# Performance work log

Measured on AMD Instinct MI355X. Metric: run time of the kernel, lower is better.

The kernel has to match this reference:

```python
import jax, jax.numpy as jnp
import numpy as np

B, C, T = 8, 8, 2048
WIN = 512
F_BINS = WIN // 2 + 1  # 257
H, NH = 256, 4
DH = H // NH
EPS = 1e-4


def _ln(x, g, b):
    m = jnp.mean(x, -1, keepdims=True)
    v = jnp.var(x, -1, keepdims=True)
    return (x - m) / jnp.sqrt(v + 1e-5) * g + b


def setup_inputs() -> dict:
    key = jax.random.key(0)
    ks = jax.random.split(key, 16)
    w = lambda i, shape: jax.random.normal(ks[i], shape, jnp.float32) * 0.02
    return {
        'x': jax.random.normal(ks[0], (B, C, T, F_BINS), jnp.float32),
        'W_in': w(1, (F_BINS, H)), 'b_in': jnp.zeros((H,), jnp.float32),
        'W_out': w(2, (H, F_BINS)), 'b_out': jnp.zeros((F_BINS,), jnp.float32),
        'Wq': w(3, (H, H)), 'bq': jnp.zeros((H,), jnp.float32),
        'Wk': w(4, (H, H)), 'bk': jnp.zeros((H,), jnp.float32),
        'Wv': w(5, (H, H)), 'bv': jnp.zeros((H,), jnp.float32),
        'Wo': w(6, (H, H)), 'bo': jnp.zeros((H,), jnp.float32),
        'ln1_g': jnp.ones((H,), jnp.float32), 'ln1_b': jnp.zeros((H,), jnp.float32),
        'Wf1': w(7, (H, WIN)), 'bf1': jnp.zeros((WIN,), jnp.float32),
        'Wf2': w(8, (WIN, H)), 'bf2': jnp.zeros((H,), jnp.float32),
        'ln2_g': jnp.ones((H,), jnp.float32), 'ln2_b': jnp.zeros((H,), jnp.float32),
        'Ws1': w(9, (H, H // 2)), 'bs1': jnp.zeros((H // 2,), jnp.float32),
        'Ws2': w(10, (H // 2, 1)), 'bs2': jnp.zeros((1,), jnp.float32),
        'ps_a': jnp.zeros((1,), jnp.float32), 'ps_b': jnp.ones((1,), jnp.float32),
    }


def _forward(x, W_in, b_in, W_out, b_out, Wq, bq, Wk, bk, Wv, bv, Wo, bo,
             ln1_g, ln1_b, Wf1, bf1, Wf2, bf2, ln2_g, ln2_b,
             Ws1, bs1, Ws2, bs2, ps_a, ps_b):
    lin1 = jax.nn.relu(x @ W_in + b_in)  # [B,C,T,H]
    b, c, t, h_dim = lin1.shape

    def encoder(q, kv):
        # q: [B,T,H], kv: [B,Cc,T,H]; per-time-frame attention over channels
        cc = kv.shape[1]
        Q = (q @ Wq + bq).reshape(b, t, NH, DH)
        K = (kv @ Wk + bk).reshape(b, cc, t, NH, DH)
        V = (kv @ Wv + bv).reshape(b, cc, t, NH, DH)
        scores = jnp.einsum('bthd,bcthd->bthc', Q, K) / jnp.sqrt(jnp.float32(DH))
        A = jax.nn.softmax(scores, axis=-1)
        ctx = jnp.einsum('bthc,bcthd->bthd', A, V).reshape(b, t, h_dim)
        h1 = _ln(q + ctx @ Wo + bo, ln1_g, ln1_b)
        f = jax.nn.relu(h1 @ Wf1 + bf1) @ Wf2 + bf2
        return _ln(h1 + f, ln2_g, ln2_b)

    def seen_enough(hh):
        s = jax.nn.relu(hh @ Ws1 + bs1) @ Ws2 + bs2
        return jax.nn.sigmoid((s - ps_a) / (ps_b + 1e-8))

    still = jnp.ones((b, t, 1), jnp.float32)
    cum = jnp.zeros((b, t, 1), jnp.float32)
    rem = jnp.ones((b, t, 1), jnp.float32)
    pc = jnp.zeros((b, t, 1), jnp.float32)
    out = jnp.zeros((b, t, h_dim), jnp.float32)
    gate = jnp.float32(1.0)  # replicates data-dependent early break

    for ci in range(c):  # small fixed loop over mic channels (ACT ponder)
        hh = encoder(lin1[:, ci], lin1[:, :ci + 1])
        cur = seen_enough(hh) if ci < c - 1 else jnp.ones((b, t, 1), jnp.float32)
        cum_n = cum + cur * still
        pc_n = pc + still
        still_n = (cum_n < 1 - EPS).astype(jnp.float32)
        out_n = out + hh * (cur * still_n + rem * (1 - still_n))
        rem_n = rem - cur * still_n
        pc_n = pc_n + rem_n * (1 - still_n)
        live = gate > 0.5
        cum = jnp.where(live, cum_n, cum)
        pc = jnp.where(live, pc_n, pc)
        out = jnp.where(live, out_n, out)
        rem = jnp.where(live, rem_n, rem)
        still = jnp.where(live, still_n, still)
        gate = gate * (jnp.sum(still) >= EPS).astype(jnp.float32)

    encoder_out = jax.nn.relu(out @ W_out + b_out)  # [B,T,F]
    return encoder_out, pc[:, :, 0]


def reference(x, W_in, b_in, W_out, b_out, Wq, bq, Wk, bk, Wv, bv, Wo, bo,
              ln1_g, ln1_b, Wf1, bf1, Wf2, bf2, ln2_g, ln2_b,
              Ws1, bs1, Ws2, bs2, ps_a, ps_b):
    return _forward(x, W_in, b_in, W_out, b_out, Wq, bq, Wk, bk, Wv, bv, Wo, bo,
                    ln1_g, ln1_b, Wf1, bf1, Wf2, bf2, ln2_g, ln2_b,
                    Ws1, bs1, Ws2, bs2, ps_a, ps_b)
```

## Files before the change

### kernel.cpp

```cpp
#include <hip/hip_runtime.h>
#include <hip/hip_bf16.h>
#include <math.h>

typedef _Float16 f16;
typedef _Float16 f16x4 __attribute__((ext_vector_type(4)));
typedef _Float16 f16x8 __attribute__((ext_vector_type(8)));
typedef float f32x16 __attribute__((ext_vector_type(16)));

constexpr int CH = 8;
constexpr int TT = 2048;
constexpr int FB = 257;
constexpr int HD = 256;
constexpr int DHD = 64;
constexpr int WN = 512;
constexpr int HF = 128;
constexpr int RR = 8 * TT;
constexpr int KXP = 288;

#define MFMA3(ACCV, AH, AL, BH, BL)                                            \
  ACCV = __builtin_amdgcn_mfma_f32_32x32x16_f16(AL, BH, ACCV, 0, 0, 0);        \
  ACCV = __builtin_amdgcn_mfma_f32_32x32x16_f16(AH, BL, ACCV, 0, 0, 0);        \
  ACCV = __builtin_amdgcn_mfma_f32_32x32x16_f16(AH, BH, ACCV, 0, 0, 0);

template<int ACT>
__global__ __launch_bounds__(256, 2) void gemm2(
    const f16* __restrict__ Ahi, const f16* __restrict__ Alo, int K,
    const f16* __restrict__ Bp, const float* __restrict__ bias,
    float* __restrict__ C0, int ldc, int Nreal)
{
  __shared__ f16 As[2][2][128][40];
  const int tid = threadIdx.x;
  const int m0 = blockIdx.x * 128;
  const int n0 = blockIdx.y * 64;
  const int q = tid & 3, r = tid >> 2;
  const int lane = tid & 63, wm = tid >> 6;
  const int lr = lane & 31, lg = lane >> 5;
  const int nb0 = n0 >> 5, kd8 = K >> 3;

  f32x16 acc[2];
  #pragma unroll
  for (int nf = 0; nf < 2; nf++)
    #pragma unroll
    for (int g = 0; g < 16; g++) acc[nf][g] = 0.f;

  const long aoff = (long)(m0 + r) * K + q * 8;
  const long hstep = (long)64 * K;
  f16x8 sA[4];
  auto loadA = [&](int k0) {
    const long a = aoff + k0;
    sA[0] = *(const f16x8*)(Ahi + a);  sA[1] = *(const f16x8*)(Ahi + a + hstep);
    sA[2] = *(const f16x8*)(Alo + a);  sA[3] = *(const f16x8*)(Alo + a + hstep);
  };
  auto loadB = [&](f16x8 B[2][2][2], int k0) {
    const int kb = (k0 >> 3) + lg;
    #pragma unroll
    for (int kh = 0; kh < 2; kh++)
      #pragma unroll
      for (int nf = 0; nf < 2; nf++)
        #pragma unroll
        for (int hl = 0; hl < 2; hl++)
          B[kh][nf][hl] = *(const f16x8*)(Bp +
              ((long)((nb0 + nf) * kd8 + kb + kh * 2) * 512 + hl * 256 + lr * 8));
  };
  auto kstep = [&](f16x8 SB[2][2][2], f16x8 TB[2][2][2], int k0, int d) {
    *(f16x8*)&As[d][0][r][q * 8]      = sA[0];
    *(f16x8*)&As[d][0][r + 64][q * 8] = sA[1];
    *(f16x8*)&As[d][1][r][q * 8]      = sA[2];
    *(f16x8*)&As[d][1][r + 64][q * 8] = sA[3];
    __syncthreads();
    if (k0 + 32 < K) { loadA(k0 + 32); loadB(TB, k0 + 32); }
    f16x8 fa[2][2];
    #pragma unroll
    for (int kh = 0; kh < 2; kh++)
      #pragma unroll
      for (int hl = 0; hl < 2; hl++)
        fa[kh][hl] = *(const f16x8*)&As[d][hl][wm * 32 + lr][kh * 16 + lg * 8];
    #pragma unroll
    for (int kh = 0; kh < 2; kh++)
      #pragma unroll
      for (int nf = 0; nf < 2; nf++) {
        MFMA3(acc[nf], fa[kh][0], fa[kh][1], SB[kh][nf][0], SB[kh][nf][1]);
      }
  };

  f16x8 B0[2][2][2], B1[2][2][2];
  loadA(0);
  loadB(B0, 0);
  int d = 0;
  for (int k0 = 0; k0 < K; k0 += 64) {
    kstep(B0, B1, k0, d); d ^= 1;
    if (k0 + 32 < K) { kstep(B1, B0, k0 + 32, d); d ^= 1; }
  }

  #pragma unroll
  for (int nf = 0; nf < 2; nf++) {
    const int col = n0 + nf * 32 + lr;
    const float bb = (col < Nreal) ? bias[col] : 0.f;
    #pragma unroll
    for (int g = 0; g < 16; g++) {
      const long row = m0 + wm * 32 + (g & 3) + 8 * (g >> 2) + 4 * lg;
      float v = acc[nf][g] + bb;
      if (ACT) v = fmaxf(v, 0.f);
      if (col < Nreal) C0[row * (long)ldc + col] = v;
    }
  }
}

__global__ __launch_bounds__(512) void lin1_qkv(
    const float* __restrict__ x, long agrp,
    const f16* __restrict__ WinP, const float* __restrict__ b_in,
    const f16* __restrict__ WqkvP, const float* __restrict__ bq,
    const float* __restrict__ bk, const float* __restrict__ bv,
    f16* __restrict__ lin1hi, f16* __restrict__ lin1lo,
    float* __restrict__ Qb, float* __restrict__ Ksd, float* __restrict__ Vsd,
    const int* __restrict__ alive)
{
  if (alive && *alive == 0) return;
  __shared__ f16 As[2][2][64][40];
  __shared__ f16 L1[2][64][264];
  const int tid = threadIdx.x;
  const int m0 = blockIdx.x * 64;
  const int lane = tid & 63, wave = tid >> 6;
  const int wm = wave & 1, wn = wave >> 1;
  const int lr = lane & 31, lg = lane >> 5;
  const int srow = tid >> 3, sk = (tid & 7) * 4;

  const int r0 = m0 + srow;
  const float* xrow = x + (long)(r0 >> 11) * agrp + (long)(r0 & 2047) * FB;

  f16x4 sAh, sAl;
  auto loadA = [&](int k0) {
    float v[4];
    #pragma unroll
    for (int j = 0; j < 4; j++) {
      const int k = k0 + sk + j;
      v[j] = (k < FB) ? xrow[k] : 0.f;
    }
    #pragma unroll
    for (int j = 0; j < 4; j++) {
      const f16 h = (f16)v[j];
      sAh[j] = h; sAl[j] = (f16)(v[j] - (float)h);
    }
  };
  auto loadB1 = [&](f16x8 B[2][2][2], int k0) {
    const int kb = (k0 >> 3) + lg;
    #pragma unroll
    for (int kh = 0; kh < 2; kh++)
      #pragma unroll
      for (int nf = 0; nf < 2; nf++)
        #pragma unroll
        for (int hl = 0; hl < 2; hl++)
          B[kh][nf][hl] = *(const f16x8*)(WinP +
              ((long)((wn * 2 + nf) * 36 + kb + kh * 2) * 512 + hl * 256 + lr * 8));
  };

  f32x16 acc[2];
  #pragma unroll
  for (int nf = 0; nf < 2; nf++)
    #pragma unroll
    for (int g = 0; g < 16; g++) acc[nf][g] = 0.f;

  auto kstep1 = [&](f16x8 SB[2][2][2], f16x8 TB[2][2][2], int k0, int d) {
    *(f16x4*)&As[d][0][srow][sk] = sAh;
    *(f16x4*)&As[d][1][srow][sk] = sAl;
    __syncthreads();
    if (k0 + 32 < KXP) { loadA(k0 + 32); loadB1(TB, k0 + 32); }
    f16x8 fa[2][2];
    #pragma unroll
    for (int kh = 0; kh < 2; kh++)
      #pragma unroll
      for (int hl = 0; hl < 2; hl++)
        fa[kh][hl] = *(const f16x8*)&As[d][hl][wm * 32 + lr][kh * 16 + lg * 8];
    #pragma unroll
    for (int kh = 0; kh < 2; kh++)
      #pragma unroll
      for (int nf = 0; nf < 2; nf++) {
        MFMA3(acc[nf], fa[kh][0], fa[kh][1], SB[kh][nf][0], SB[kh][nf][1]);
      }
  };

  f16x8 B0[2][2][2], B1[2][2][2];
  loadA(0);
  loadB1(B0, 0);
  #pragma unroll
  for (int s = 0; s < 9; s++) {
    if ((s & 1) == 0) kstep1(B0, B1, s * 32, 0);
    else              kstep1(B1, B0, s * 32, 1);
  }

  #pragma unroll
  for (int nf = 0; nf < 2; nf++) {
    const int col = wn * 64 + nf * 32 + lr;
    const float bb = b_in[col];
    #pragma unroll
    for (int g = 0; g < 16; g++) {
      const int row_l = wm * 32 + (g & 3) + 8 * (g >> 2) + 4 * lg;
      const float v = fmaxf(acc[nf][g] + bb, 0.f);
      const f16 hi = (f16)v;
      const f16 lo = (f16)(v - (float)hi);
      L1[0][row_l][col] = hi;
      L1[1][row_l][col] = lo;
      const long gi = (long)(m0 + row_l) * HD + col;
      lin1hi[gi] = hi;
      lin1lo[gi] = lo;
    }
  }
  __syncthreads();

  auto loadB2 = [&](f16x8 B[2][2][2], int k0, int sel) {
    const int kb = (k0 >> 3) + lg;
    #pragma unroll
    for (int kh = 0; kh < 2; kh++)
      #pragma unroll
      for (int nf = 0; nf < 2; nf++)
        #pragma unroll
        for (int hl = 0; hl < 2; hl++)
          B[kh][nf][hl] = *(const f16x8*)(WqkvP +
              ((long)((sel * 8 + wn * 2 + nf) * 32 + kb + kh * 2) * 512 + hl * 256 + lr * 8));
  };
  #pragma unroll
  for (int sel = 0; sel < 3; sel++) {
    f32x16 a2[2];
    #pragma unroll
    for (int nf = 0; nf < 2; nf++)
      #pragma unroll
      for (int g = 0; g < 16; g++) a2[nf][g] = 0.f;
    f16x8 Bc[2][2][2], Bn[2][2][2];
    loadB2(Bc, 0, sel);
    #pragma unroll
    for (int s = 0; s < 8; s++) {
      const int k0 = s * 32;
      if (s < 7) loadB2((s & 1) ? Bc : Bn, k0 + 32, sel);
      f16x8 fa[2][2];
      #pragma unroll
      for (int kh = 0; kh < 2; kh++)
        #pragma unroll
        for (int hl = 0; hl < 2; hl++)
          fa[kh][hl] = *(const f16x8*)&L1[hl][wm * 32 + lr][k0 + kh * 16 + lg * 8];
      #pragma unroll
      for (int kh = 0; kh < 2; kh++)
        #pragma unroll
        for (int nf = 0; nf < 2; nf++) {
          if (s & 1) { MFMA3(a2[nf], fa[kh][0], fa[kh][1], Bn[kh][nf][0], Bn[kh][nf][1]); }
          else       { MFMA3(a2[nf], fa[kh][0], fa[kh][1], Bc[kh][nf][0], Bc[kh][nf][1]); }
        }
    }
    float* dst = sel == 0 ? Qb : (sel == 1 ? Ksd : Vsd);
    const float* bp = sel == 0 ? bq : (sel == 1 ? bk : bv);
    #pragma unroll
    for (int nf = 0; nf < 2; nf++) {
      const int col = wn * 64 + nf * 32 + lr;
      const float bb = bp[col];
      #pragma unroll
      for (int g = 0; g < 16; g++) {
        const int row_l = wm * 32 + (g & 3) + 8 * (g >> 2) + 4 * lg;
        dst[(long)(m0 + row_l) * HD + col] = a2[nf][g] + bb;
      }
    }
  }
}

__global__ __launch_bounds__(512) void ffn_ln(
    const f16* __restrict__ h1hi, const f16* __restrict__ h1lo,
    const f16* __restrict__ Wf1P, const float* __restrict__ bf1,
    const f16* __restrict__ Wf2P, const float* __restrict__ bf2,
    const float* __restrict__ g2, const float* __restrict__ b2,
    f16* __restrict__ hhhi, f16* __restrict__ hhlo,
    const int* __restrict__ alive)
{
  if (alive && *alive == 0) return;
  __shared__ f16 H1[2][64][264];
  __shared__ f16 T1[2][64][264];
  __shared__ float red[64][4][2];
  const int tid = threadIdx.x;
  const int m0 = blockIdx.x * 64;
  const int lane = tid & 63, wave = tid >> 6;
  const int wm = wave & 1, wn = wave >> 1;
  const int lr = lane & 31, lg = lane >> 5;

  {
    const int srow = tid >> 3, scg = (tid & 7) * 32;
    const long hb = (long)(m0 + srow) * HD + scg;
    #pragma unroll
    for (int j = 0; j < 4; j++) {
      *(f16x8*)&H1[0][srow][scg + j * 8] = *(const f16x8*)(h1hi + hb + j * 8);
      *(f16x8*)&H1[1][srow][scg + j * 8] = *(const f16x8*)(h1lo + hb + j * 8);
    }
  }
  __syncthreads();

  auto loadBf1 = [&](f16x8 B[2][2][2], int k0, int p) {
    const int kb = (k0 >> 3) + lg;
    #pragma unroll
    for (int kh = 0; kh < 2; kh++)
      #pragma unroll
      for (int nf = 0; nf < 2; nf++)
        #pragma unroll
        for (int hl = 0; hl < 2; hl++)
          B[kh][nf][hl] = *(const f16x8*)(Wf1P +
              ((long)((p * 8 + wn * 2 + nf) * 32 + kb + kh * 2) * 512 + hl * 256 + lr * 8));
  };
  auto loadBf2 = [&](f16x8 B[2][2][2], int k0, int p) {
    const int kb = p * 32 + (k0 >> 3) + lg;
    #pragma unroll
    for (int kh = 0; kh < 2; kh++)
      #pragma unroll
      for (int nf = 0; nf < 2; nf++)
        #pragma unroll
        for (int hl = 0; hl < 2; hl++)
          B[kh][nf][hl] = *(const f16x8*)(Wf2P +
              ((long)((wn * 2 + nf) * 64 + kb + kh * 2) * 512 + hl * 256 + lr * 8));
  };

  f32x16 hacc[2];
  #pragma unroll
  for (int nf = 0; nf < 2; nf++)
    #pragma unroll
    for (int g = 0; g < 16; g++) hacc[nf][g] = 0.f;

  #pragma unroll
  for (int p = 0; p < 2; p++) {
    f32x16 ta[2];
    #pragma unroll
    for (int nf = 0; nf < 2; nf++)
      #pragma unroll
      for (int g = 0; g < 16; g++) ta[nf][g] = 0.f;
    {
      f16x8 Bc[2][2][2], Bn[2][2][2];
      loadBf1(Bc, 0, p);
      #pragma unroll
      for (int s = 0; s < 8; s++) {
        const int k0 = s * 32;
        if (s < 7) loadBf1((s & 1) ? Bc : Bn, k0 + 32, p);
        f16x8 fa[2][2];
        #pragma unroll
        for (int kh = 0; kh < 2; kh++)
          #pragma unroll
          for (int hl = 0; hl < 2; hl++)
            fa[kh][hl] = *(const f16x8*)&H1[hl][wm * 32 + lr][k0 + kh * 16 + lg * 8];
        #pragma unroll
        for (int kh = 0; kh < 2; kh++)
          #pragma unroll
          for (int nf = 0; nf < 2; nf++) {
            if (s & 1) { MFMA3(ta[nf], fa[kh][0], fa[kh][1], Bn[kh][nf][0], Bn[kh][nf][1]); }
            else       { MFMA3(ta[nf], fa[kh][0], fa[kh][1], Bc[kh][nf][0], Bc[kh][nf][1]); }
          }
      }
    }
    __syncthreads();
    #pragma unroll
    for (int nf = 0; nf < 2; nf++) {
      const int col = wn * 64 + nf * 32 + lr;
      const float bb = bf1[p * 256 + col];
      #pragma unroll
      for (int g = 0; g < 16; g++) {
        const int row_l = wm * 32 + (g & 3) + 8 * (g >> 2) + 4 * lg;
        const float v = fmaxf(ta[nf][g] + bb, 0.f);
        const f16 hi = (f16)v;
        T1[0][row_l][col] = hi;
        T1[1][row_l][col] = (f16)(v - (float)hi);
      }
    }
    __syncthreads();
    {
      f16x8 Bc[2][2][2], Bn[2][2][2];
      loadBf2(Bc, 0, p);
      #pragma unroll
      for (int s = 0; s < 8; s++) {
        const int k0 = s * 32;
        if (s < 7) loadBf2((s & 1) ? Bc : Bn, k0 + 32, p);
        f16x8 ft[2][2];
        #pragma unroll
        for (int kh = 0; kh < 2; kh++)
          #pragma unroll
          for (int hl = 0; hl < 2; hl++)
            ft[kh][hl] = *(const f16x8*)&T1[hl][wm * 32 + lr][k0 + kh * 16 + lg * 8];
        #pragma unroll
        for (int kh = 0; kh < 2; kh++)
          #pragma unroll
          for (int nf = 0; nf < 2; nf++) {
            if (s & 1) { MFMA3(hacc[nf], ft[kh][0], ft[kh][1], Bn[kh][nf][0], Bn[kh][nf][1]); }
            else       { MFMA3(hacc[nf], ft[kh][0], ft[kh][1], Bc[kh][nf][0], Bc[kh][nf][1]); }
          }
      }
    }
  }

  float pr[16], qr[16];
  #pragma unroll
  for (int g = 0; g < 16; g++) {
    const int row_l = wm * 32 + (g & 3) + 8 * (g >> 2) + 4 * lg;
    float s = 0.f, sq = 0.f;
    #pragma unroll
    for (int nf = 0; nf < 2; nf++) {
      const int col = wn * 64 + nf * 32 + lr;
      float v = hacc[nf][g] + bf2[col]
              + (float)H1[0][row_l][col] + (float)H1[1][row_l][col];
      hacc[nf][g] = v;
      s += v; sq += v * v;
    }
    pr[g] = s; qr[g] = sq;
  }
  #pragma unroll
  for (int g = 0; g < 16; g++)
    #pragma unroll
    for (int i = 1; i <= 16; i <<= 1) {
      pr[g] += __shfl_xor(pr[g], i, 64);
      qr[g] += __shfl_xor(qr[g], i, 64);
    }
  if (lr == 0) {
    #pragma unroll
    for (int g = 0; g < 16; g++) {
      const int row_l = wm * 32 + (g & 3) + 8 * (g >> 2) + 4 * lg;
      red[row_l][wn][0] = pr[g];
      red[row_l][wn][1] = qr[g];
    }
  }
  __syncthreads();
  #pragma unroll
  for (int g = 0; g < 16; g++) {
    const int row_l = wm * 32 + (g & 3) + 8 * (g >> 2) + 4 * lg;
    const float mean = (red[row_l][0][0] + red[row_l][1][0] +
                        red[row_l][2][0] + red[row_l][3][0]) * (1.f / HD);
    const float ex2 = (red[row_l][0][1] + red[row_l][1][1] +
                       red[row_l][2][1] + red[row_l][3][1]) * (1.f / HD);
    const float inv = 1.f / sqrtf(ex2 - mean * mean + 1e-5f);
    const long rbase = (long)(m0 + row_l) * HD;
    #pragma unroll
    for (int nf = 0; nf < 2; nf++) {
      const int col = wn * 64 + nf * 32 + lr;
      const float o = (hacc[nf][g] - mean) * inv * g2[col] + b2[col];
      const f16 hi = (f16)o;
      hhhi[rbase + col] = hi;
      hhlo[rbase + col] = (f16)(o - (float)hi);
    }
  }
}

__global__ __launch_bounds__(512) void gemm_ln(
    const f16* __restrict__ Ahi, const f16* __restrict__ Alo, int K,
    const f16* __restrict__ Bp, const float* __restrict__ bias,
    const f16* __restrict__ Rhi, const f16* __restrict__ Rlo,
    const float* __restrict__ gg, const float* __restrict__ bb_,
    f16* __restrict__ Ohi, f16* __restrict__ Olo,
    const int* __restrict__ alive)
{
  if (alive && *alive == 0) return;
  __shared__ f16 As[2][2][64][40];
  __shared__ float red[64][4][2];
  const int tid = threadIdx.x;
  const int m0 = blockIdx.x * 64;
  const int lane = tid & 63, wave = tid >> 6;
  const int wm = wave & 1, wn = wave >> 1;
  const int lr = lane & 31, lg = lane >> 5;
  const int srow = tid >> 3, sk = (tid & 7) * 4;
  const int kd8 = K >> 3;

  f32x16 acc[2];
  #pragma unroll
  for (int nf = 0; nf < 2; nf++)
    #pragma unroll
    for (int g = 0; g < 16; g++) acc[nf][g] = 0.f;

  const f16* arh = Ahi + (long)(m0 + srow) * K + sk;
  const f16* arl = Alo + (long)(m0 + srow) * K + sk;
  f16x4 sAh, sAl;
  auto loadA = [&](int k0) {
    sAh = *(const f16x4*)(arh + k0);
    sAl = *(const f16x4*)(arl + k0);
  };
  auto loadB = [&](f16x8 B[2][2][2], int k0) {
    const int kb = (k0 >> 3) + lg;
    #pragma unroll
    for (int kh = 0; kh < 2; kh++)
      #pragma unroll
      for (int nf = 0; nf < 2; nf++)
        #pragma unroll
        for (int hl = 0; hl < 2; hl++)
          B[kh][nf][hl] = *(const f16x8*)(Bp +
              ((long)((wn * 2 + nf) * kd8 + kb + kh * 2) * 512 + hl * 256 + lr * 8));
  };
  auto kstep = [&](f16x8 SB[2][2][2], f16x8 TB[2][2][2], int k0, int d) {
    *(f16x4*)&As[d][0][srow][sk] = sAh;
    *(f16x4*)&As[d][1][srow][sk] = sAl;
    __syncthreads();
    if (k0 + 32 < K) { loadA(k0 + 32); loadB(TB, k0 + 32); }
    f16x8 fa[2][2];
    #pragma unroll
    for (int kh = 0; kh < 2; kh++)
      #pragma unroll
      for (int hl = 0; hl < 2; hl++)
        fa[kh][hl] = *(const f16x8*)&As[d][hl][wm * 32 + lr][kh * 16 + lg * 8];
    #pragma unroll
    for (int kh = 0; kh < 2; kh++)
      #pragma unroll
      for (int nf = 0; nf < 2; nf++) {
        MFMA3(acc[nf], fa[kh][0], fa[kh][1], SB[kh][nf][0], SB[kh][nf][1]);
      }
  };

  f16x8 B0[2][2][2], B1[2][2][2];
  loadA(0);
  loadB(B0, 0);
  int d = 0;
  for (int k0 = 0; k0 < K; k0 += 64) {
    kstep(B0, B1, k0, d); d ^= 1;
    if (k0 + 32 < K) { kstep(B1, B0, k0 + 32, d); d ^= 1; }
  }

  float pr[16], qr[16];
  #pragma unroll
  for (int g = 0; g < 16; g++) {
    const int row_l = wm * 32 + (g & 3) + 8 * (g >> 2) + 4 * lg;
    const long rbase = (long)(m0 + row_l) * HD;
    float s = 0.f, sq = 0.f;
    #pragma unroll
    for (int nf = 0; nf < 2; nf++) {
      const int col = wn * 64 + nf * 32 + lr;
      float v = acc[nf][g] + bias[col]
              + (float)Rhi[rbase + col] + (float)Rlo[rbase + col];
      acc[nf][g] = v;
      s += v; sq += v * v;
    }
    pr[g] = s; qr[g] = sq;
  }
  #pragma unroll
  for (int g = 0; g < 16; g++)
    #pragma unroll
    for (int i = 1; i <= 16; i <<= 1) {
      pr[g] += __shfl_xor(pr[g], i, 64);
      qr[g] += __shfl_xor(qr[g], i, 64);
    }
  if (lr == 0) {
    #pragma unroll
    for (int g = 0; g < 16; g++) {
      const int row_l = wm * 32 + (g & 3) + 8 * (g >> 2) + 4 * lg;
      red[row_l][wn][0] = pr[g];
      red[row_l][wn][1] = qr[g];
    }
  }
  __syncthreads();
  #pragma unroll
  for (int g = 0; g < 16; g++) {
    const int row_l = wm * 32 + (g & 3) + 8 * (g >> 2) + 4 * lg;
    const float mean = (red[row_l][0][0] + red[row_l][1][0] +
                        red[row_l][2][0] + red[row_l][3][0]) * (1.f / HD);
    const float ex2 = (red[row_l][0][1] + red[row_l][1][1] +
                       red[row_l][2][1] + red[row_l][3][1]) * (1.f / HD);
    const float inv = 1.f / sqrtf(ex2 - mean * mean + 1e-5f);
    const long rbase = (long)(m0 + row_l) * HD;
    #pragma unroll
    for (int nf = 0; nf < 2; nf++) {
      const int col = wn * 64 + nf * 32 + lr;
      const float o = (acc[nf][g] - mean) * inv * gg[col] + bb_[col];
      const f16 hi = (f16)o;
      Ohi[rbase + col] = hi;
      Olo[rbase + col] = (f16)(o - (float)hi);
    }
  }
}

template<int FIRST>
__global__ __launch_bounds__(256) void s1_act(
    const f16* __restrict__ hhhi, const f16* __restrict__ hhlo,
    const f16* __restrict__ Bp, const float* __restrict__ bs1,
    const float* __restrict__ Ws2, const float* __restrict__ bs2,
    const float* __restrict__ psa, const float* __restrict__ psb,
    float* __restrict__ cum, float* __restrict__ rem,
    float* __restrict__ still, float* __restrict__ pc,
    f16* __restrict__ outhi, f16* __restrict__ outlo,
    float* __restrict__ pcdst,
    const int* __restrict__ alive, int* __restrict__ myFlag)
{
  if (!FIRST && alive && *alive == 0) return;
  __shared__ f16 As[2][2][64][40];
  __shared__ float red[64][2];
  const int tid = threadIdx.x;
  const int m0 = blockIdx.x * 64;
  const int lane = tid & 63, wave = tid >> 6;
  const int wm = wave & 1, wn = wave >> 1;
  const int lr = lane & 31, lg = lane >> 5;
  const int srow = tid >> 2, sk = (tid & 3) * 8;
  const int K = HD, kd8 = K >> 3;

  f32x16 acc[2];
  #pragma unroll
  for (int nf = 0; nf < 2; nf++)
    #pragma unroll
    for (int g = 0; g < 16; g++) acc[nf][g] = 0.f;

  const f16* arh = hhhi + (long)(m0 + srow) * K + sk;
  const f16* arl = hhlo + (long)(m0 + srow) * K + sk;
  f16x8 sAh, sAl;
  auto loadA = [&](int k0) {
    sAh = *(const f16x8*)(arh + k0);
    sAl = *(const f16x8*)(arl + k0);
  };
  auto loadB = [&](f16x8 B[2][2][2], int k0) {
    const int kb = (k0 >> 3) + lg;
    #pragma unroll
    for (int kh = 0; kh < 2; kh++)
      #pragma unroll
      for (int nf = 0; nf < 2; nf++)
        #pragma unroll
        for (int hl = 0; hl < 2; hl++)
          B[kh][nf][hl] = *(const f16x8*)(Bp +
              ((long)((wn * 2 + nf) * kd8 + kb + kh * 2) * 512 + hl * 256 + lr * 8));
  };
  auto kstep = [&](f16x8 SB[2][2][2], f16x8 TB[2][2][2], int k0, int d) {
    *(f16x8*)&As[d][0][srow][sk] = sAh;
    *(f16x8*)&As[d][1][srow][sk] = sAl;
    __syncthreads();
    if (k0 + 32 < K) { loadA(k0 + 32); loadB(TB, k0 + 32); }
    f16x8 fa[2][2];
    #pragma unroll
    for (int kh = 0; kh < 2; kh++)
      #pragma unroll
      for (int hl = 0; hl < 2; hl++)
        fa[kh][hl] = *(const f16x8*)&As[d][hl][wm * 32 + lr][kh * 16 + lg * 8];
    #pragma unroll
    for (int kh = 0; kh < 2; kh++)
      #pragma unroll
      for (int nf = 0; nf < 2; nf++) {
        MFMA3(acc[nf], fa[kh][0], fa[kh][1], SB[kh][nf][0], SB[kh][nf][1]);
      }
  };

  f16x8 B0[2][2][2], B1[2][2][2];
  loadA(0);
  loadB(B0, 0);
  int d = 0;
  for (int k0 = 0; k0 < K; k0 += 64) {
    kstep(B0, B1, k0, d); d ^= 1;
    if (k0 + 32 < K) { kstep(B1, B0, k0 + 32, d); d ^= 1; }
  }

  float pr[16];
  #pragma unroll
  for (int g = 0; g < 16; g++) {
    float s = 0.f;
    #pragma unroll
    for (int nf = 0; nf < 2; nf++) {
      const int col = wn * 64 + nf * 32 + lr;
      const float v = fmaxf(acc[nf][g] + bs1[col], 0.f);
      s += v * Ws2[col];
    }
    pr[g] = s;
  }
  #pragma unroll
  for (int g = 0; g < 16; g++)
    #pragma unroll
    for (int i = 1; i <= 16; i <<= 1) pr[g] += __shfl_xor(pr[g], i, 64);
  if (lr == 0) {
    #pragma unroll
    for (int g = 0; g < 16; g++) {
      const int row_l = wm * 32 + (g & 3) + 8 * (g >> 2) + 4 * lg;
      red[row_l][wn] = pr[g];
    }
  }
  __syncthreads();

  const float ipsb = 1.f / (psb[0] + 1e-8f);
  const float pa = psa[0], b2v = bs2[0];
  for (int row_l = 0; row_l < 64; row_l++) {
    const long rg = m0 + row_l;
    const float s = red[row_l][0] + red[row_l][1] + b2v;
    const float curv = 1.f / (1.f + expf(-(s - pa) * ipsb));
    const float cu = FIRST ? 0.f : cum[rg];
    const float re = FIRST ? 1.f : rem[rg];
    const float st = FIRST ? 1.f : still[rg];
    const float pp = FIRST ? 0.f : pc[rg];
    const float cum_n = cu + curv * st;
    float pc_n = pp + st;
    const float still_n = (cum_n < 0.9999f) ? 1.f : 0.f;
    const float wgt = curv * still_n + re * (1.f - still_n);
    const long idx = rg * HD + tid;
    const float prev = FIRST ? 0.f : ((float)outhi[idx] + (float)outlo[idx]);
    const float hhv = (float)hhhi[idx] + (float)hhlo[idx];
    const float newv = prev + hhv * wgt;
    const f16 hi = (f16)newv;
    outhi[idx] = hi;
    outlo[idx] = (f16)(newv - (float)hi);
    const float rem_n = re - curv * still_n;
    pc_n += rem_n * (1.f - still_n);
    if (tid == 0) {
      cum[rg] = cum_n; rem[rg] = rem_n; still[rg] = still_n; pc[rg] = pc_n;
      pcdst[rg] = pc_n;
      if (still_n > 0.5f) *myFlag = 1;
    }
  }
}

__global__ __launch_bounds__(256) void act_last(
    const f16* __restrict__ hhhi, const f16* __restrict__ hhlo,
    float* __restrict__ cum, float* __restrict__ rem,
    float* __restrict__ still, float* __restrict__ pc,
    f16* __restrict__ outhi, f16* __restrict__ outlo,
    float* __restrict__ pcdst, const int* __restrict__ alive)
{
  if (alive && *alive == 0) return;
  const int tid = threadIdx.x;
  for (int rr = 0; rr < 8; rr++) {
    const long r = (long)blockIdx.x * 8 + rr;
    const float re = rem[r], st = still[r];
    const float cum_n = cum[r] + st;
    float pc_n = pc[r] + st;
    const float still_n = (cum_n < 0.9999f) ? 1.f : 0.f;
    const float wgt = still_n + re * (1.f - still_n);
    const long idx = r * HD + tid;
    const float newv = (float)outhi[idx] + (float)outlo[idx]
                     + ((float)hhhi[idx] + (float)hhlo[idx]) * wgt;
    const f16 hi = (f16)newv;
    outhi[idx] = hi;
    outlo[idx] = (f16)(newv - (float)hi);
    const float rem_n = re - still_n;
    pc_n += rem_n * (1.f - still_n);
    if (tid == 0) {
      cum[r] = cum_n; rem[r] = rem_n; still[r] = still_n; pc[r] = pc_n;
      pcdst[r] = pc_n;
    }
  }
}

__global__ __launch_bounds__(256) void wsplit_k(
    const float* __restrict__ W_in, const float* __restrict__ Wq,
    const float* __restrict__ Wk, const float* __restrict__ Wv,
    const float* __restrict__ Wo, const float* __restrict__ Wf1,
    const float* __restrict__ Wf2, const float* __restrict__ Ws1,
    const float* __restrict__ Wout,
    f16* __restrict__ WinP, f16* __restrict__ WqkvP, f16* __restrict__ WoP,
    f16* __restrict__ Wf1P, f16* __restrict__ Wf2P, f16* __restrict__ Ws1P,
    f16* __restrict__ WoutP)
{
  const int y = blockIdx.y;
  const long idx = (long)blockIdx.x * 256 + threadIdx.x;
  int Npad, Kpad, Ksrc;
  f16* dst;
  switch (y) {
    case 0: Npad = 256; Kpad = 288; Ksrc = 257; dst = WinP;  break;
    case 1: Npad = 768; Kpad = 256; Ksrc = 256; dst = WqkvP; break;
    case 2: Npad = 256; Kpad = 256; Ksrc = 256; dst = WoP;   break;
    case 3: Npad = 512; Kpad = 256; Ksrc = 256; dst = Wf1P;  break;
    case 4: Npad = 256; Kpad = 512; Ksrc = 512; dst = Wf2P;  break;
    case 5: Npad = 128; Kpad = 256; Ksrc = 256; dst = Ws1P;  break;
    default: Npad = 384; Kpad = 256; Ksrc = 256; dst = WoutP; break;
  }
  if (idx >= (long)Npad * Kpad) return;
  const int n = (int)(idx / Kpad), k = (int)(idx % Kpad);
  float v = 0.f;
  if (k < Ksrc) {
    switch (y) {
      case 0: v = W_in[(long)k * 256 + n]; break;
      case 1: { const int sel = n >> 8;
                const float* s = sel == 0 ? Wq : (sel == 1 ? Wk : Wv);
                v = s[(long)k * 256 + (n & 255)]; } break;
      case 2: v = Wo[(long)k * 256 + n]; break;
      case 3: v = Wf1[(long)k * 512 + n]; break;
      case 4: v = Wf2[(long)k * 256 + n]; break;
      case 5: v = Ws1[(long)k * 128 + n]; break;
      default: v = (n < 257) ? Wout[(long)k * 257 + n] : 0.f; break;
    }
  }
  const long base = ((long)(n >> 5) * (Kpad >> 3) + (k >> 3)) * 512 + (n & 31) * 8 + (k & 7);
  const f16 hi = (f16)v;
  dst[base] = hi;
  dst[base + 256] = (f16)(v - (float)hi);
}

template<int NCc>
__global__ __launch_bounds__(256) void attn_k(
    const float* __restrict__ Q, const float* __restrict__ Ksp,
    const float* __restrict__ Vsp, f16* __restrict__ chi,
    f16* __restrict__ clo, const int* __restrict__ alive)
{
  if (alive && *alive == 0) return;
  const int w = threadIdx.x >> 6;
  const int l = threadIdx.x & 63;
  for (int rr = 0; rr < 4; rr++) {
    const long r = (long)blockIdx.x * 4 + rr;
    const float qv = Q[r * HD + w * DHD + l];
    float sc[NCc];
    #pragma unroll
    for (int c = 0; c < NCc; c++) {
      float p = qv * Ksp[((long)c * RR + r) * HD + w * DHD + l];
      #pragma unroll
      for (int s = 32; s > 0; s >>= 1) p += __shfl_xor(p, s, 64);
      sc[c] = p * 0.125f;
    }
    float m = sc[0];
    #pragma unroll
    for (int c = 1; c < NCc; c++) m = fmaxf(m, sc[c]);
    float a[NCc];
    float den = 0.f;
    #pragma unroll
    for (int c = 0; c < NCc; c++) { a[c] = expf(sc[c] - m); den += a[c]; }
    float cv = 0.f;
    #pragma unroll
    for (int c = 0; c < NCc; c++)
      cv = fmaf(a[c] / den, Vsp[((long)c * RR + r) * HD + w * DHD + l], cv);
    const f16 hi = (f16)cv;
    chi[r * HD + w * DHD + l] = hi;
    clo[r * HD + w * DHD + l] = (f16)(cv - (float)hi);
  }
}

__global__ void init_k(int* flags) {
  if (threadIdx.x < 8) flags[threadIdx.x] = 0;
}

extern "C" void kernel_launch(void* const* d_in, const int* in_sizes, int n_in,
                              void* d_out, int out_size, void* d_ws, size_t ws_size,
                              hipStream_t stream) {
  const float* x    = (const float*)d_in[0];
  const float* W_in = (const float*)d_in[1];
  const float* b_in = (const float*)d_in[2];
  const float* W_out= (const float*)d_in[3];
  const float* b_out= (const float*)d_in[4];
  const float* Wq   = (const float*)d_in[5];
  const float* bq   = (const float*)d_in[6];
  const float* Wk   = (const float*)d_in[7];
  const float* bk   = (const float*)d_in[8];
  const float* Wv   = (const float*)d_in[9];
  const float* bv   = (const float*)d_in[10];
  const float* Wo   = (const float*)d_in[11];
  const float* bo   = (const float*)d_in[12];
  const float* ln1g = (const float*)d_in[13];
  const float* ln1b = (const float*)d_in[14];
  const float* Wf1  = (const float*)d_in[15];
  const float* bf1  = (const float*)d_in[16];
  const float* Wf2  = (const float*)d_in[17];
  const float* bf2  = (const float*)d_in[18];
  const float* ln2g = (const float*)d_in[19];
  const float* ln2b = (const float*)d_in[20];
  const float* Ws1  = (const float*)d_in[21];
  const float* bs1  = (const float*)d_in[22];
  const float* Ws2  = (const float*)d_in[23];
  const float* bs2  = (const float*)d_in[24];
  const float* psa  = (const float*)d_in[25];
  const float* psb  = (const float*)d_in[26];

  float* ws = (float*)d_ws;
  long off = 0;
  auto alloc = [&](long n) { float* p = ws + off; off += n; return p; };
  float* Ks   = alloc((long)CH * RR * HD);
  float* Vs   = alloc((long)CH * RR * HD);
  float* Qb   = alloc((long)RR * HD);
  f16* lin1hi = (f16*)alloc((long)RR * HD / 2);
  f16* lin1lo = (f16*)alloc((long)RR * HD / 2);
  f16* ctxhi  = (f16*)alloc((long)RR * HD / 2);
  f16* ctxlo  = (f16*)alloc((long)RR * HD / 2);
  f16* h1hi   = (f16*)alloc((long)RR * HD / 2);
  f16* h1lo   = (f16*)alloc((long)RR * HD / 2);
  f16* hhhi   = (f16*)alloc((long)RR * HD / 2);
  f16* hhlo   = (f16*)alloc((long)RR * HD / 2);
  f16* outhi  = (f16*)alloc((long)RR * HD / 2);
  f16* outlo  = (f16*)alloc((long)RR * HD / 2);
  f16* WinP   = (f16*)alloc(2 * 256 * 288 / 2);
  f16* WqkvP  = (f16*)alloc(2 * 768 * 256 / 2);
  f16* WoP    = (f16*)alloc(2 * 256 * 256 / 2);
  f16* Wf1P   = (f16*)alloc(2 * 512 * 256 / 2);
  f16* Wf2P   = (f16*)alloc(2 * 256 * 512 / 2);
  f16* Ws1P   = (f16*)alloc(2 * 128 * 256 / 2);
  f16* WoutP  = (f16*)alloc(2 * 384 * 256 / 2);
  float* cum  = alloc(RR);
  float* rem  = alloc(RR);
  float* still= alloc(RR);
  float* pc   = alloc(RR);
  int* flags  = (int*)alloc(8);

  init_k<<<1, 256, 0, stream>>>(flags);
  wsplit_k<<<dim3(768, 7), 256, 0, stream>>>(
      W_in, Wq, Wk, Wv, Wo, Wf1, Wf2, Ws1, W_out,
      WinP, WqkvP, WoP, Wf1P, Wf2P, Ws1P, WoutP);

  float* pcdst = (float*)d_out + (long)RR * FB;

  for (int ci = 0; ci < CH; ci++) {
    const int* al = (ci == 0) ? nullptr : (flags + ci - 1);
    lin1_qkv<<<256, 512, 0, stream>>>(
        x + (long)ci * TT * FB, (long)CH * TT * FB,
        WinP, b_in, WqkvP, bq, bk, bv,
        lin1hi, lin1lo, Qb,
        Ks + (long)ci * RR * HD, Vs + (long)ci * RR * HD, al);
    switch (ci) {
      case 0: attn_k<1><<<4096, 256, 0, stream>>>(Qb, Ks, Vs, ctxhi, ctxlo, al); break;
      case 1: attn_k<2><<<4096, 256, 0, stream>>>(Qb, Ks, Vs, ctxhi, ctxlo, al); break;
      case 2: attn_k<3><<<4096, 256, 0, stream>>>(Qb, Ks, Vs, ctxhi, ctxlo, al); break;
      case 3: attn_k<4><<<4096, 256, 0, stream>>>(Qb, Ks, Vs, ctxhi, ctxlo, al); break;
      case 4: attn_k<5><<<4096, 256, 0, stream>>>(Qb, Ks, Vs, ctxhi, ctxlo, al); break;
      case 5: attn_k<6><<<4096, 256, 0, stream>>>(Qb, Ks, Vs, ctxhi, ctxlo, al); break;
      case 6: attn_k<7><<<4096, 256, 0, stream>>>(Qb, Ks, Vs, ctxhi, ctxlo, al); break;
      default: attn_k<8><<<4096, 256, 0, stream>>>(Qb, Ks, Vs, ctxhi, ctxlo, al); break;
    }
    gemm_ln<<<256, 512, 0, stream>>>(
        ctxhi, ctxlo, HD, WoP, bo, lin1hi, lin1lo, ln1g, ln1b,
        h1hi, h1lo, al);
    ffn_ln<<<256, 512, 0, stream>>>(
        h1hi, h1lo, Wf1P, bf1, Wf2P, bf2, ln2g, ln2b, hhhi, hhlo, al);
    if (ci == 0)
      s1_act<1><<<256, 256, 0, stream>>>(
          hhhi, hhlo, Ws1P, bs1, Ws2, bs2, psa, psb,
          cum, rem, still, pc, outhi, outlo, pcdst, nullptr, flags + 0);
    else if (ci < CH - 1)
      s1_act<0><<<256, 256, 0, stream>>>(
          hhhi, hhlo, Ws1P, bs1, Ws2, bs2, psa, psb,
          cum, rem, still, pc, outhi, outlo, pcdst, al, flags + ci);
    else
      act_last<<<2048, 256, 0, stream>>>(
          hhhi, hhlo, cum, rem, still, pc, outhi, outlo, pcdst, al);
  }
  gemm2<1><<<dim3(128, 6), 256, 0, stream>>>(
      outhi, outlo, HD, WoutP, b_out, (float*)d_out, FB, FB);
}
```

Before: 749.7 us.

## Fuse attention into Wo+LN kernel and FFN+LN into the halting-score kernel

Attention over channels is now computed inside the Wo projection kernel and written straight to shared memory, so the ctx hi/lo buffers and their global round trip are gone. The FFN+LayerNorm kernel is merged with the halting-score GEMM and accumulation step, and keeps the hh result in shared memory instead of writing and rereading hhhi/hhlo. This removes two to three launches per channel iteration and several activation round trips. The cost is that attention runs only 256 blocks with a serial 32-row loop per wave, and the larger fused kernels may raise register and LDS pressure.

New measurement: 811.9 us. +8.3%, slower.

```diff
diff --git a/kernel.cpp b/kernel.cpp
--- a/kernel.cpp
+++ b/kernel.cpp
@@ -260,36 +260,71 @@
   }
 }
 
-__global__ __launch_bounds__(512) void ffn_ln(
-    const f16* __restrict__ h1hi, const f16* __restrict__ h1lo,
-    const f16* __restrict__ Wf1P, const float* __restrict__ bf1,
-    const f16* __restrict__ Wf2P, const float* __restrict__ bf2,
-    const float* __restrict__ g2, const float* __restrict__ b2,
-    f16* __restrict__ hhhi, f16* __restrict__ hhlo,
+template<int NCc>
+__global__ __launch_bounds__(512) void attn_wo_ln(
+    const float* __restrict__ Qb, const float* __restrict__ Ksp,
+    const float* __restrict__ Vsp,
+    const f16* __restrict__ WoP, const float* __restrict__ bo,
+    const f16* __restrict__ Rhi, const f16* __restrict__ Rlo,
+    const float* __restrict__ gg, const float* __restrict__ bb_,
+    f16* __restrict__ Ohi, f16* __restrict__ Olo,
     const int* __restrict__ alive)
 {
   if (alive && *alive == 0) return;
-  __shared__ f16 H1[2][64][264];
-  __shared__ f16 T1[2][64][264];
+  __shared__ f16 C1[2][64][264];
   __shared__ float red[64][4][2];
   const int tid = threadIdx.x;
   const int m0 = blockIdx.x * 64;
   const int lane = tid & 63, wave = tid >> 6;
+
+  {
+    const int h = wave & 3;
+    const int rbase = (wave >> 2) * 32;
+    for (int i = 0; i < 32; i++) {
+      const int row_l = rbase + i;
+      const long r = m0 + row_l;
+      const long qi = r * HD + h * DHD + lane;
+      const float qv = Qb[qi];
+      float kv[NCc], vv[NCc];
+      #pragma unroll
+      for (int c = 0; c < NCc; c++) {
+        kv[c] = Ksp[((long)c * RR + r) * HD + h * DHD + lane];
+        vv[c] = Vsp[((long)c * RR + r) * HD + h * DHD + lane];
+      }
+      float sc[NCc];
+      #pragma unroll
+      for (int c = 0; c < NCc; c++) {
+        float p = qv * kv[c];
+        #pragma unroll
+        for (int s = 32; s > 0; s >>= 1) p += __shfl_xor(p, s, 64);
+        sc[c] = p * 0.125f;
+      }
+      float m = sc[0];
+      #pragma unroll
+      for (int c = 1; c < NCc; c++) m = fmaxf(m, sc[c]);
+      float a[NCc];
+      float den = 0.f;
+      #pragma unroll
+      for (int c = 0; c < NCc; c++) { a[c] = expf(sc[c] - m); den += a[c]; }
+      float cv = 0.f;
+      #pragma unroll
+      for (int c = 0; c < NCc; c++) cv = fmaf(a[c] / den, vv[c], cv);
+      const f16 hi = (f16)cv;
+      C1[0][row_l][h * DHD + lane] = hi;
+      C1[1][row_l][h * DHD + lane] = (f16)(cv - (float)hi);
+    }
+  }
+  __syncthreads();
+
   const int wm = wave & 1, wn = wave >> 1;
   const int lr = lane & 31, lg = lane >> 5;
-
-  {
-    const int srow = tid >> 3, scg = (tid & 7) * 32;
-    const long hb = (long)(m0 + srow) * HD + scg;
-    #pragma unroll
-    for (int j = 0; j < 4; j++) {
-      *(f16x8*)&H1[0][srow][scg + j * 8] = *(const f16x8*)(h1hi + hb + j * 8);
-      *(f16x8*)&H1[1][srow][scg + j * 8] = *(const f16x8*)(h1lo + hb + j * 8);
-    }
-  }
-  __syncthreads();
-
-  auto loadBf1 = [&](f16x8 B[2][2][2], int k0, int p) {
+  f32x16 acc[2];
+  #pragma unroll
+  for (int nf = 0; nf < 2; nf++)
+    #pragma unroll
+    for (int g = 0; g < 16; g++) acc[nf][g] = 0.f;
+
+  auto loadB = [&](f16x8 B[2][2][2], int k0) {
     const int kb = (k0 >> 3) + lg;
     #pragma unroll
     for (int kh = 0; kh < 2; kh++)
@@ -297,106 +332,42 @@
       for (int nf = 0; nf < 2; nf++)
         #pragma unroll
         for (int hl = 0; hl < 2; hl++)
-          B[kh][nf][hl] = *(const f16x8*)(Wf1P +
-              ((long)((p * 8 + wn * 2 + nf) * 32 + kb + kh * 2) * 512 + hl * 256 + lr * 8));
-  };
-  auto loadBf2 = [&](f16x8 B[2][2][2], int k0, int p) {
-    const int kb = p * 32 + (k0 >> 3) + lg;
-    #pragma unroll
-    for (int kh = 0; kh < 2; kh++)
-      #pragma unroll
-      for (int nf = 0; nf < 2; nf++)
-        #pragma unroll
-        for (int hl = 0; hl < 2; hl++)
-          B[kh][nf][hl] = *(const f16x8*)(Wf2P +
-              ((long)((wn * 2 + nf) * 64 + kb + kh * 2) * 512 + hl * 256 + lr * 8));
-  };
-
-  f32x16 hacc[2];
-  #pragma unroll
-  for (int nf = 0; nf < 2; nf++)
-    #pragma unroll
-    for (int g = 0; g < 16; g++) hacc[nf][g] = 0.f;
-
-  #pragma unroll
-  for (int p = 0; p < 2; p++) {
-    f32x16 ta[2];
-    #pragma unroll
-    for (int nf = 0; nf < 2; nf++)
-      #pragma unroll
-      for (int g = 0; g < 16; g++) ta[nf][g] = 0.f;
-    {
-      f16x8 Bc[2][2][2], Bn[2][2][2];
-      loadBf1(Bc, 0, p);
-      #pragma unroll
-      for (int s = 0; s < 8; s++) {
-        const int k0 = s * 32;
-        if (s < 7) loadBf1((s & 1) ? Bc : Bn, k0 + 32, p);
-        f16x8 fa[2][2];
-        #pragma unroll
-        for (int kh = 0; kh < 2; kh++)
-          #pragma unroll
-          for (int hl = 0; hl < 2; hl++)
-            fa[kh][hl] = *(const f16x8*)&H1[hl][wm * 32 + lr][k0 + kh * 16 + lg * 8];
-        #pragma unroll
-        for (int kh = 0; kh < 2; kh++)
-          #pragma unroll
-          for (int nf = 0; nf < 2; nf++) {
-            if (s & 1) { MFMA3(ta[nf], fa[kh][0], fa[kh][1], Bn[kh][nf][0], Bn[kh][nf][1]); }
-            else       { MFMA3(ta[nf], fa[kh][0], fa[kh][1], Bc[kh][nf][0], Bc[kh][nf][1]); }
-          }
-      }
-    }
-    __syncthreads();
+          B[kh][nf][hl] = *(const f16x8*)(WoP +
+              ((long)((wn * 2 + nf) * 32 + kb + kh * 2) * 512 + hl * 256 + lr * 8));
+  };
+  f16x8 Bc[2][2][2], Bn[2][2][2];
+  loadB(Bc, 0);
+  #pragma unroll
+  for (int s = 0; s < 8; s++) {
+    const int k0 = s * 32;
+    if (s < 7) loadB((s & 1) ? Bc : Bn, k0 + 32);
+    f16x8 fa[2][2];
+    #pragma unroll
+    for (int kh = 0; kh < 2; kh++)
+      #pragma unroll
+      for (int hl = 0; hl < 2; hl++)
+        fa[kh][hl] = *(const f16x8*)&C1[hl][wm * 32 + lr][k0 + kh * 16 + lg * 8];
+    #pragma unroll
+    for (int kh = 0; kh < 2; kh++)
+      #pragma unroll
+      for (int nf = 0; nf < 2; nf++) {
+        if (s & 1) { MFMA3(acc[nf], fa[kh][0], fa[kh][1], Bn[kh][nf][0], Bn[kh][nf][1]); }
+        else       { MFMA3(acc[nf], fa[kh][0], fa[kh][1], Bc[kh][nf][0], Bc[kh][nf][1]); }
+      }
+  }
+
+  float pr[16], qr[16];
+  #pragma unroll
+  for (int g = 0; g < 16; g++) {
+    const int row_l = wm * 32 + (g & 3) + 8 * (g >> 2) + 4 * lg;
+    const long rbase = (long)(m0 + row_l) * HD;
+    float s = 0.f, sq = 0.f;
     #pragma unroll
     for (int nf = 0; nf < 2; nf++) {
       const int col = wn * 64 + nf * 32 + lr;
-      const float bb = bf1[p * 256 + col];
-      #pragma unroll
-      for (int g = 0; g < 16; g++) {
-        const int row_l = wm * 32 + (g & 3) + 8 * (g >> 2) + 4 * lg;
-        const float v = fmaxf(ta[nf][g] + bb, 0.f);
-        const f16 hi = (f16)v;
-        T1[0][row_l][col] = hi;
-        T1[1][row_l][col] = (f16)(v - (float)hi);
-      }
-    }
-    __syncthreads();
-    {
-      f16x8 Bc[2][2][2], Bn[2][2][2];
-      loadBf2(Bc, 0, p);
-      #pragma unroll
-      for (int s = 0; s < 8; s++) {
-        const int k0 = s * 32;
-        if (s < 7) loadBf2((s & 1) ? Bc : Bn, k0 + 32, p);
-        f16x8 ft[2][2];
-        #pragma unroll
-        for (int kh = 0; kh < 2; kh++)
-          #pragma unroll
-          for (int hl = 0; hl < 2; hl++)
-            ft[kh][hl] = *(const f16x8*)&T1[hl][wm * 32 + lr][k0 + kh * 16 + lg * 8];
-        #pragma unroll
-        for (int kh = 0; kh < 2; kh++)
-          #pragma unroll
-          for (int nf = 0; nf < 2; nf++) {
-            if (s & 1) { MFMA3(hacc[nf], ft[kh][0], ft[kh][1], Bn[kh][nf][0], Bn[kh][nf][1]); }
-            else       { MFMA3(hacc[nf], ft[kh][0], ft[kh][1], Bc[kh][nf][0], Bc[kh][nf][1]); }
-          }
-      }
-    }
-  }
-
-  float pr[16], qr[16];
-  #pragma unroll
-  for (int g = 0; g < 16; g++) {
-    const int row_l = wm * 32 + (g & 3) + 8 * (g >> 2) + 4 * lg;
-    float s = 0.f, sq = 0.f;
-    #pragma unroll
-    for (int nf = 0; nf < 2; nf++) {
-      const int col = wn * 64 + nf * 32 + lr;
-      float v = hacc[nf][g] + bf2[col]
-              + (float)H1[0][row_l][col] + (float)H1[1][row_l][col];
-      hacc[nf][g] = v;
+      float v = acc[nf][g] + bo[col]
+              + (float)Rhi[rbase + col] + (float)Rlo[rbase + col];
+      acc[nf][g] = v;
       s += v; sq += v * v;
     }
     pr[g] = s; qr[g] = sq;
@@ -429,129 +400,6 @@
     #pragma unroll
     for (int nf = 0; nf < 2; nf++) {
       const int col = wn * 64 + nf * 32 + lr;
-      const float o = (hacc[nf][g] - mean) * inv * g2[col] + b2[col];
-      const f16 hi = (f16)o;
-      hhhi[rbase + col] = hi;
-      hhlo[rbase + col] = (f16)(o - (float)hi);
-    }
-  }
-}
-
-__global__ __launch_bounds__(512) void gemm_ln(
-    const f16* __restrict__ Ahi, const f16* __restrict__ Alo, int K,
-    const f16* __restrict__ Bp, const float* __restrict__ bias,
-    const f16* __restrict__ Rhi, const f16* __restrict__ Rlo,
-    const float* __restrict__ gg, const float* __restrict__ bb_,
-    f16* __restrict__ Ohi, f16* __restrict__ Olo,
-    const int* __restrict__ alive)
-{
-  if (alive && *alive == 0) return;
-  __shared__ f16 As[2][2][64][40];
-  __shared__ float red[64][4][2];
-  const int tid = threadIdx.x;
-  const int m0 = blockIdx.x * 64;
-  const int lane = tid & 63, wave = tid >> 6;
-  const int wm = wave & 1, wn = wave >> 1;
-  const int lr = lane & 31, lg = lane >> 5;
-  const int srow = tid >> 3, sk = (tid & 7) * 4;
-  const int kd8 = K >> 3;
-
-  f32x16 acc[2];
-  #pragma unroll
-  for (int nf = 0; nf < 2; nf++)
-    #pragma unroll
-    for (int g = 0; g < 16; g++) acc[nf][g] = 0.f;
-
-  const f16* arh = Ahi + (long)(m0 + srow) * K + sk;
-  const f16* arl = Alo + (long)(m0 + srow) * K + sk;
-  f16x4 sAh, sAl;
-  auto loadA = [&](int k0) {
-    sAh = *(const f16x4*)(arh + k0);
-    sAl = *(const f16x4*)(arl + k0);
-  };
-  auto loadB = [&](f16x8 B[2][2][2], int k0) {
-    const int kb = (k0 >> 3) + lg;
-    #pragma unroll
-    for (int kh = 0; kh < 2; kh++)
-      #pragma unroll
-      for (int nf = 0; nf < 2; nf++)
-        #pragma unroll
-        for (int hl = 0; hl < 2; hl++)
-          B[kh][nf][hl] = *(const f16x8*)(Bp +
-              ((long)((wn * 2 + nf) * kd8 + kb + kh * 2) * 512 + hl * 256 + lr * 8));
-  };
-  auto kstep = [&](f16x8 SB[2][2][2], f16x8 TB[2][2][2], int k0, int d) {
-    *(f16x4*)&As[d][0][srow][sk] = sAh;
-    *(f16x4*)&As[d][1][srow][sk] = sAl;
-    __syncthreads();
-    if (k0 + 32 < K) { loadA(k0 + 32); loadB(TB, k0 + 32); }
-    f16x8 fa[2][2];
-    #pragma unroll
-    for (int kh = 0; kh < 2; kh++)
-      #pragma unroll
-      for (int hl = 0; hl < 2; hl++)
-        fa[kh][hl] = *(const f16x8*)&As[d][hl][wm * 32 + lr][kh * 16 + lg * 8];
-    #pragma unroll
-    for (int kh = 0; kh < 2; kh++)
-      #pragma unroll
-      for (int nf = 0; nf < 2; nf++) {
-        MFMA3(acc[nf], fa[kh][0], fa[kh][1], SB[kh][nf][0], SB[kh][nf][1]);
-      }
-  };
-
-  f16x8 B0[2][2][2], B1[2][2][2];
-  loadA(0);
-  loadB(B0, 0);
-  int d = 0;
-  for (int k0 = 0; k0 < K; k0 += 64) {
-    kstep(B0, B1, k0, d); d ^= 1;
-    if (k0 + 32 < K) { kstep(B1, B0, k0 + 32, d); d ^= 1; }
-  }
-
-  float pr[16], qr[16];
-  #pragma unroll
-  for (int g = 0; g < 16; g++) {
-    const int row_l = wm * 32 + (g & 3) + 8 * (g >> 2) + 4 * lg;
-    const long rbase = (long)(m0 + row_l) * HD;
-    float s = 0.f, sq = 0.f;
-    #pragma unroll
-    for (int nf = 0; nf < 2; nf++) {
-      const int col = wn * 64 + nf * 32 + lr;
-      float v = acc[nf][g] + bias[col]
-              + (float)Rhi[rbase + col] + (float)Rlo[rbase + col];
-      acc[nf][g] = v;
-      s += v; sq += v * v;
-    }
-    pr[g] = s; qr[g] = sq;
-  }
-  #pragma unroll
-  for (int g = 0; g < 16; g++)
-    #pragma unroll
-    for (int i = 1; i <= 16; i <<= 1) {
-      pr[g] += __shfl_xor(pr[g], i, 64);
-      qr[g] += __shfl_xor(qr[g], i, 64);
-    }
-  if (lr == 0) {
-    #pragma unroll
-    for (int g = 0; g < 16; g++) {
-      const int row_l = wm * 32 + (g & 3) + 8 * (g >> 2) + 4 * lg;
-      red[row_l][wn][0] = pr[g];
-      red[row_l][wn][1] = qr[g];
-    }
-  }
-  __syncthreads();
-  #pragma unroll
-  for (int g = 0; g < 16; g++) {
-    const int row_l = wm * 32 + (g & 3) + 8 * (g >> 2) + 4 * lg;
-    const float mean = (red[row_l][0][0] + red[row_l][1][0] +
-                        red[row_l][2][0] + red[row_l][3][0]) * (1.f / HD);
-    const float ex2 = (red[row_l][0][1] + red[row_l][1][1] +
-                       red[row_l][2][1] + red[row_l][3][1]) * (1.f / HD);
-    const float inv = 1.f / sqrtf(ex2 - mean * mean + 1e-5f);
-    const long rbase = (long)(m0 + row_l) * HD;
-    #pragma unroll
-    for (int nf = 0; nf < 2; nf++) {
-      const int col = wn * 64 + nf * 32 + lr;
       const float o = (acc[nf][g] - mean) * inv * gg[col] + bb_[col];
       const f16 hi = (f16)o;
       Ohi[rbase + col] = hi;
@@ -560,10 +408,13 @@
   }
 }
 
-template<int FIRST>
-__global__ __launch_bounds__(256) void s1_act(
-    const f16* __restrict__ hhhi, const f16* __restrict__ hhlo,
-    const f16* __restrict__ Bp, const float* __restrict__ bs1,
+template<int MODE>
+__global__ __launch_bounds__(512) void ffn_act(
+    const f16* __restrict__ h1hi, const f16* __restrict__ h1lo,
+    const f16* __restrict__ Wf1P, const float* __restrict__ bf1,
+    const f16* __restrict__ Wf2P, const float* __restrict__ bf2,
+    const float* __restrict__ g2, const float* __restrict__ b2,
+    const f16* __restrict__ Ws1P, const float* __restrict__ bs1,
     const float* __restrict__ Ws2, const float* __restrict__ bs2,
     const float* __restrict__ psa, const float* __restrict__ psb,
     float* __restrict__ cum, float* __restrict__ rem,
@@ -572,152 +423,273 @@
     float* __restrict__ pcdst,
     const int* __restrict__ alive, int* __restrict__ myFlag)
 {
-  if (!FIRST && alive && *alive == 0) return;
-  __shared__ f16 As[2][2][64][40];
-  __shared__ float red[64][2];
+  if (MODE != 0 && alive && *alive == 0) return;
+  __shared__ f16 H1[2][64][264];
+  __shared__ f16 T1[2][64][264];
+  __shared__ float red[64][4][2];
+  __shared__ float red2[64][2];
   const int tid = threadIdx.x;
   const int m0 = blockIdx.x * 64;
   const int lane = tid & 63, wave = tid >> 6;
   const int wm = wave & 1, wn = wave >> 1;
   const int lr = lane & 31, lg = lane >> 5;
-  const int srow = tid >> 2, sk = (tid & 3) * 8;
-  const int K = HD, kd8 = K >> 3;
-
-  f32x16 acc[2];
+
+  {
+    const int srow = tid >> 3, scg = (tid & 7) * 32;
+    const long hb = (long)(m0 + srow) * HD + scg;
+    #pragma unroll
+    for (int j = 0; j < 4; j++) {
+      *(f16x8*)&H1[0][srow][scg + j * 8] = *(const f16x8*)(h1hi + hb + j * 8);
+      *(f16x8*)&H1[1][srow][scg + j * 8] = *(const f16x8*)(h1lo + hb + j * 8);
+    }
+  }
+  __syncthreads();
+
+  auto loadBf1 = [&](f16x8 B[2][2][2], int k0, int p) {
+    const int kb = (k0 >> 3) + lg;
+    #pragma unroll
+    for (int kh = 0; kh < 2; kh++)
+      #pragma unroll
+      for (int nf = 0; nf < 2; nf++)
+        #pragma unroll
+        for (int hl = 0; hl < 2; hl++)
+          B[kh][nf][hl] = *(const f16x8*)(Wf1P +
+              ((long)((p * 8 + wn * 2 + nf) * 32 + kb + kh * 2) * 512 + hl * 256 + lr * 8));
+  };
+  auto loadBf2 = [&](f16x8 B[2][2][2], int k0, int p) {
+    const int kb = p * 32 + (k0 >> 3) + lg;
+    #pragma unroll
+    for (int kh = 0; kh < 2; kh++)
+      #pragma unroll
+      for (int nf = 0; nf < 2; nf++)
+        #pragma unroll
+        for (int hl = 0; hl < 2; hl++)
+          B[kh][nf][hl] = *(const f16x8*)(Wf2P +
+              ((long)((wn * 2 + nf) * 64 + kb + kh * 2) * 512 + hl * 256 + lr * 8));
+  };
+
+  f32x16 hacc[2];
   #pragma unroll
   for (int nf = 0; nf < 2; nf++)
     #pragma unroll
-    for (int g = 0; g < 16; g++) acc[nf][g] = 0.f;
-
-  const f16* arh = hhhi + (long)(m0 + srow) * K + sk;
-  const f16* arl = hhlo + (long)(m0 + srow) * K + sk;
-  f16x8 sAh, sAl;
-  auto loadA = [&](int k0) {
-    sAh = *(const f16x8*)(arh + k0);
-    sAl = *(const f16x8*)(arl + k0);
-  };
-  auto loadB = [&](f16x8 B[2][2][2], int k0) {
-    const int kb = (k0 >> 3) + lg;
-    #pragma unroll
-    for (int kh = 0; kh < 2; kh++)
-      #pragma unroll
-      for (int nf = 0; nf < 2; nf++)
-        #pragma unroll
-        for (int hl = 0; hl < 2; hl++)
-          B[kh][nf][hl] = *(const f16x8*)(Bp +
-              ((long)((wn * 2 + nf) * kd8 + kb + kh * 2) * 512 + hl * 256 + lr * 8));
-  };
-  auto kstep = [&](f16x8 SB[2][2][2], f16x8 TB[2][2][2], int k0, int d) {
-    *(f16x8*)&As[d][0][srow][sk] = sAh;
-    *(f16x8*)&As[d][1][srow][sk] = sAl;
+    for (int g = 0; g < 16; g++) hacc[nf][g] = 0.f;
+
+  #pragma unroll
+  for (int p = 0; p < 2; p++) {
+    f32x16 ta[2];
+    #pragma unroll
+    for (int nf = 0; nf < 2; nf++)
+      #pragma unroll
+      for (int g = 0; g < 16; g++) ta[nf][g] = 0.f;
+    {
+      f16x8 Bc[2][2][2], Bn[2][2][2];
+      loadBf1(Bc, 0, p);
+      #pragma unroll
+      for (int s = 0; s < 8; s++) {
+        const int k0 = s * 32;
+        if (s < 7) loadBf1((s & 1) ? Bc : Bn, k0 + 32, p);
+        f16x8 fa[2][2];
+        #pragma unroll
+        for (int kh = 0; kh < 2; kh++)
+          #pragma unroll
+          for (int hl = 0; hl < 2; hl++)
+            fa[kh][hl] = *(const f16x8*)&H1[hl][wm * 32 + lr][k0 + kh * 16 + lg * 8];
+        #pragma unroll
+        for (int kh = 0; kh < 2; kh++)
+          #pragma unroll
+          for (int nf = 0; nf < 2; nf++) {
+            if (s & 1) { MFMA3(ta[nf], fa[kh][0], fa[kh][1], Bn[kh][nf][0], Bn[kh][nf][1]); }
+            else       { MFMA3(ta[nf], fa[kh][0], fa[kh][1], Bc[kh][nf][0], Bc[kh][nf][1]); }
+          }
+      }
+    }
     __syncthreads();
-    if (k0 + 32 < K) { loadA(k0 + 32); loadB(TB, k0 + 32); }
-    f16x8 fa[2][2];
-    #pragma unroll
-    for (int kh = 0; kh < 2; kh++)
-      #pragma unroll
-      for (int hl = 0; hl < 2; hl++)
-        fa[kh][hl] = *(const f16x8*)&As[d][hl][wm * 32 + lr][kh * 16 + lg * 8];
-    #pragma unroll
-    for (int kh = 0; kh < 2; kh++)
-      #pragma unroll
-      for (int nf = 0; nf < 2; nf++) {
-        MFMA3(acc[nf], fa[kh][0], fa[kh][1], SB[kh][nf][0], SB[kh][nf][1]);
-      }
-  };
-
-  f16x8 B0[2][2][2], B1[2][2][2];
-  loadA(0);
-  loadB(B0, 0);
-  int d = 0;
-  for (int k0 = 0; k0 < K; k0 += 64) {
-    kstep(B0, B1, k0, d); d ^= 1;
-    if (k0 + 32 < K) { kstep(B1, B0, k0 + 32, d); d ^= 1; }
-  }
-
-  float pr[16];
-  #pragma unroll
-  for (int g = 0; g < 16; g++) {
-    float s = 0.f;
     #pragma unroll
     for (int nf = 0; nf < 2; nf++) {
       const int col = wn * 64 + nf * 32 + lr;
-      const float v = fmaxf(acc[nf][g] + bs1[col], 0.f);
-      s += v * Ws2[col];
-    }
-    pr[g] = s;
+      const float bb = bf1[p * 256 + col];
+      #pragma unroll
+      for (int g = 0; g < 16; g++) {
+        const int row_l = wm * 32 + (g & 3) + 8 * (g >> 2) + 4 * lg;
+        const float v = fmaxf(ta[nf][g] + bb, 0.f);
+        const f16 hi = (f16)v;
+        T1[0][row_l][col] = hi;
+        T1[1][row_l][col] = (f16)(v - (float)hi);
+      }
+    }
+    __syncthreads();
+    {
+      f16x8 Bc[2][2][2], Bn[2][2][2];
+      loadBf2(Bc, 0, p);
+      #pragma unroll
+      for (int s = 0; s < 8; s++) {
+        const int k0 = s * 32;
+        if (s < 7) loadBf2((s & 1) ? Bc : Bn, k0 + 32, p);
+        f16x8 ft[2][2];
+        #pragma unroll
+        for (int kh = 0; kh < 2; kh++)
+          #pragma unroll
+          for (int hl = 0; hl < 2; hl++)
+            ft[kh][hl] = *(const f16x8*)&T1[hl][wm * 32 + lr][k0 + kh * 16 + lg * 8];
+        #pragma unroll
+        for (int kh = 0; kh < 2; kh++)
+          #pragma unroll
+          for (int nf = 0; nf < 2; nf++) {
+            if (s & 1) { MFMA3(hacc[nf], ft[kh][0], ft[kh][1], Bn[kh][nf][0], Bn[kh][nf][1]); }
+            else       { MFMA3(hacc[nf], ft[kh][0], ft[kh][1], Bc[kh][nf][0], Bc[kh][nf][1]); }
+          }
+      }
+    }
+  }
+
+  float pr[16], qr[16];
+  #pragma unroll
+  for (int g = 0; g < 16; g++) {
+    const int row_l = wm * 32 + (g & 3) + 8 * (g >> 2) + 4 * lg;
+    float s = 0.f, sq = 0.f;
+    #pragma unroll
+    for (int nf = 0; nf < 2; nf++) {
+      const int col = wn * 64 + nf * 32 + lr;
+      float v = hacc[nf][g] + bf2[col]
+              + (float)H1[0][row_l][col] + (float)H1[1][row_l][col];
+      hacc[nf][g] = v;
+      s += v; sq += v * v;
+    }
+    pr[g] = s; qr[g] = sq;
   }
   #pragma unroll
   for (int g = 0; g < 16; g++)
     #pragma unroll
-    for (int i = 1; i <= 16; i <<= 1) pr[g] += __shfl_xor(pr[g], i, 64);
+    for (int i = 1; i <= 16; i <<= 1) {
+      pr[g] += __shfl_xor(pr[g], i, 64);
+      qr[g] += __shfl_xor(qr[g], i, 64);
+    }
   if (lr == 0) {
     #pragma unroll
     for (int g = 0; g < 16; g++) {
       const int row_l = wm * 32 + (g & 3) + 8 * (g >> 2) + 4 * lg;
-      red[row_l][wn] = pr[g];
+      red[row_l][wn][0] = pr[g];
+      red[row_l][wn][1] = qr[g];
+    }
+  }
+  __syncthreads();
+  #pragma unroll
+  for (int g = 0; g < 16; g++) {
+    const int row_l = wm * 32 + (g & 3) + 8 * (g >> 2) + 4 * lg;
+    const float mean = (red[row_l][0][0] + red[row_l][1][0] +
+                        red[row_l][2][0] + red[row_l][3][0]) * (1.f / HD);
+    const float ex2 = (red[row_l][0][1] + red[row_l][1][1] +
+                       red[row_l][2][1] + red[row_l][3][1]) * (1.f / HD);
+    const float inv = 1.f / sqrtf(ex2 - mean * mean + 1e-5f);
+    #pragma unroll
+    for (int nf = 0; nf < 2; nf++) {
+      const int col = wn * 64 + nf * 32 + lr;
+      const float o = (hacc[nf][g] - mean) * inv * g2[col] + b2[col];
+      const f16 hi = (f16)o;
+      T1[0][row_l][col] = hi;
+      T1[1][row_l][col] = (f16)(o - (float)hi);
+    }
+  }
+  __syncthreads();
+
+  if (MODE != 2) {
+    if (wave < 4) {
+      f32x16 sacc[2];
+      #pragma unroll
+      for (int nf = 0; nf < 2; nf++)
+        #pragma unroll
+        for (int g = 0; g < 16; g++) sacc[nf][g] = 0.f;
+      auto loadBs = [&](f16x8 B[2][2][2], int k0) {
+        const int kb = (k0 >> 3) + lg;
+        #pragma unroll
+        for (int kh = 0; kh < 2; kh++)
+          #pragma unroll
+          for (int nf = 0; nf < 2; nf++)
+            #pragma unroll
+            for (int hl = 0; hl < 2; hl++)
+              B[kh][nf][hl] = *(const f16x8*)(Ws1P +
+                  ((long)((wn * 2 + nf) * 32 + kb + kh * 2) * 512 + hl * 256 + lr * 8));
+      };
+      f16x8 Bc[2][2][2], Bn[2][2][2];
+      loadBs(Bc, 0);
+      #pragma unroll
+      for (int s = 0; s < 8; s++) {
+        const int k0 = s * 32;
+        if (s < 7) loadBs((s & 1) ? Bc : Bn, k0 + 32);
+        f16x8 fa[2][2];
+        #pragma unroll
+        for (int kh = 0; kh < 2; kh++)
+          #pragma unroll
+          for (int hl = 0; hl < 2; hl++)
+            fa[kh][hl] = *(const f16x8*)&T1[hl][wm * 32 + lr][k0 + kh * 16 + lg * 8];
+        #pragma unroll
+        for (int kh = 0; kh < 2; kh++)
+          #pragma unroll
+          for (int nf = 0; nf < 2; nf++) {
+            if (s & 1) { MFMA3(sacc[nf], fa[kh][0], fa[kh][1], Bn[kh][nf][0], Bn[kh][nf][1]); }
+            else       { MFMA3(sacc[nf], fa[kh][0], fa[kh][1], Bc[kh][nf][0], Bc[kh][nf][1]); }
+          }
+      }
+      float pr2[16];
+      #pragma unroll
+      for (int g = 0; g < 16; g++) {
+        float s = 0.f;
+        #pragma unroll
+        for (int nf = 0; nf < 2; nf++) {
+          const int col = wn * 64 + nf * 32 + lr;
+          const float v = fmaxf(sacc[nf][g] + bs1[col], 0.f);
+          s += v * Ws2[col];
+        }
+        pr2[g] = s;
+      }
+      #pragma unroll
+      for (int g = 0; g < 16; g++)
+        #pragma unroll
+        for (int i = 1; i <= 16; i <<= 1) pr2[g] += __shfl_xor(pr2[g], i, 64);
+      if (lr == 0) {
+        #pragma unroll
+        for (int g = 0; g < 16; g++) {
+          const int row_l = wm * 32 + (g & 3) + 8 * (g >> 2) + 4 * lg;
+          red2[row_l][wn] = pr2[g];
+        }
+      }
     }
   }
   __syncthreads();
 
   const float ipsb = 1.f / (psb[0] + 1e-8f);
   const float pa = psa[0], b2v = bs2[0];
-  for (int row_l = 0; row_l < 64; row_l++) {
+  const int colA = tid & 255, rsub = tid >> 8;
+  for (int rr = 0; rr < 32; rr++) {
+    const int row_l = rr * 2 + rsub;
     const long rg = m0 + row_l;
-    const float s = red[row_l][0] + red[row_l][1] + b2v;
-    const float curv = 1.f / (1.f + expf(-(s - pa) * ipsb));
-    const float cu = FIRST ? 0.f : cum[rg];
-    const float re = FIRST ? 1.f : rem[rg];
-    const float st = FIRST ? 1.f : still[rg];
-    const float pp = FIRST ? 0.f : pc[rg];
+    float curv;
+    if (MODE == 2) curv = 1.f;
+    else {
+      const float s = red2[row_l][0] + red2[row_l][1] + b2v;
+      curv = 1.f / (1.f + expf(-(s - pa) * ipsb));
+    }
+    const float cu = (MODE == 0) ? 0.f : cum[rg];
+    const float re = (MODE == 0) ? 1.f : rem[rg];
+    const float st = (MODE == 0) ? 1.f : still[rg];
+    const float pp = (MODE == 0) ? 0.f : pc[rg];
     const float cum_n = cu + curv * st;
     float pc_n = pp + st;
     const float still_n = (cum_n < 0.9999f) ? 1.f : 0.f;
     const float wgt = curv * still_n + re * (1.f - still_n);
-    const long idx = rg * HD + tid;
-    const float prev = FIRST ? 0.f : ((float)outhi[idx] + (float)outlo[idx]);
-    const float hhv = (float)hhhi[idx] + (float)hhlo[idx];
+    const long idx = rg * HD + colA;
+    const float prev = (MODE == 0) ? 0.f : ((float)outhi[idx] + (float)outlo[idx]);
+    const float hhv = (float)T1[0][row_l][colA] + (float)T1[1][row_l][colA];
     const float newv = prev + hhv * wgt;
     const f16 hi = (f16)newv;
     outhi[idx] = hi;
     outlo[idx] = (f16)(newv - (float)hi);
     const float rem_n = re - curv * still_n;
     pc_n += rem_n * (1.f - still_n);
-    if (tid == 0) {
+    if (colA == 0) {
       cum[rg] = cum_n; rem[rg] = rem_n; still[rg] = still_n; pc[rg] = pc_n;
       pcdst[rg] = pc_n;
-      if (still_n > 0.5f) *myFlag = 1;
-    }
-  }
-}
-
-__global__ __launch_bounds__(256) void act_last(
-    const f16* __restrict__ hhhi, const f16* __restrict__ hhlo,
-    float* __restrict__ cum, float* __restrict__ rem,
-    float* __restrict__ still, float* __restrict__ pc,
-    f16* __restrict__ outhi, f16* __restrict__ outlo,
-    float* __restrict__ pcdst, const int* __restrict__ alive)
-{
-  if (alive && *alive == 0) return;
-  const int tid = threadIdx.x;
-  for (int rr = 0; rr < 8; rr++) {
-    const long r = (long)blockIdx.x * 8 + rr;
-    const float re = rem[r], st = still[r];
-    const float cum_n = cum[r] + st;
-    float pc_n = pc[r] + st;
-    const float still_n = (cum_n < 0.9999f) ? 1.f : 0.f;
-    const float wgt = still_n + re * (1.f - still_n);
-    const long idx = r * HD + tid;
-    const float newv = (float)outhi[idx] + (float)outlo[idx]
-                     + ((float)hhhi[idx] + (float)hhlo[idx]) * wgt;
-    const f16 hi = (f16)newv;
-    outhi[idx] = hi;
-    outlo[idx] = (f16)(newv - (float)hi);
-    const float rem_n = re - still_n;
-    pc_n += rem_n * (1.f - still_n);
-    if (tid == 0) {
-      cum[r] = cum_n; rem[r] = rem_n; still[r] = still_n; pc[r] = pc_n;
-      pcdst[r] = pc_n;
+      if (MODE != 2 && still_n > 0.5f) *myFlag = 1;
     }
   }
 }
@@ -765,43 +737,6 @@
   const f16 hi = (f16)v;
   dst[base] = hi;
   dst[base + 256] = (f16)(v - (float)hi);
-}
-
-template<int NCc>
-__global__ __launch_bounds__(256) void attn_k(
-    const float* __restrict__ Q, const float* __restrict__ Ksp,
-    const float* __restrict__ Vsp, f16* __restrict__ chi,
-    f16* __restrict__ clo, const int* __restrict__ alive)
-{
-  if (alive && *alive == 0) return;
-  const int w = threadIdx.x >> 6;
-  const int l = threadIdx.x & 63;
-  for (int rr = 0; rr < 4; rr++) {
-    const long r = (long)blockIdx.x * 4 + rr;
-    const float qv = Q[r * HD + w * DHD + l];
-    float sc[NCc];
-    #pragma unroll
-    for (int c = 0; c < NCc; c++) {
-      float p = qv * Ksp[((long)c * RR + r) * HD + w * DHD + l];
-      #pragma unroll
-      for (int s = 32; s > 0; s >>= 1) p += __shfl_xor(p, s, 64);
-      sc[c] = p * 0.125f;
-    }
-    float m = sc[0];
-    #pragma unroll
-    for (int c = 1; c < NCc; c++) m = fmaxf(m, sc[c]);
-    float a[NCc];
-    float den = 0.f;
-    #pragma unroll
-    for (int c = 0; c < NCc; c++) { a[c] = expf(sc[c] - m); den += a[c]; }
-    float cv = 0.f;
-    #pragma unroll
-    for (int c = 0; c < NCc; c++)
-      cv = fmaf(a[c] / den, Vsp[((long)c * RR + r) * HD + w * DHD + l], cv);
-    const f16 hi = (f16)cv;
-    chi[r * HD + w * DHD + l] = hi;
-    clo[r * HD + w * DHD + l] = (f16)(cv - (float)hi);
-  }
 }
 
 __global__ void init_k(int* flags) {
@@ -847,12 +782,8 @@
   float* Qb   = alloc((long)RR * HD);
   f16* lin1hi = (f16*)alloc((long)RR * HD / 2);
   f16* lin1lo = (f16*)alloc((long)RR * HD / 2);
-  f16* ctxhi  = (f16*)alloc((long)RR * HD / 2);
-  f16* ctxlo  = (f16*)alloc((long)RR * HD / 2);
   f16* h1hi   = (f16*)alloc((long)RR * HD / 2);
   f16* h1lo   = (f16*)alloc((long)RR * HD / 2);
-  f16* hhhi   = (f16*)alloc((long)RR * HD / 2);
-  f16* hhlo   = (f16*)alloc((long)RR * HD / 2);
   f16* outhi  = (f16*)alloc((long)RR * HD / 2);
   f16* outlo  = (f16*)alloc((long)RR * HD / 2);
   f16* WinP   = (f16*)alloc(2 * 256 * 288 / 2);
@@ -883,31 +814,30 @@
         lin1hi, lin1lo, Qb,
         Ks + (long)ci * RR * HD, Vs + (long)ci * RR * HD, al);
     switch (ci) {
-      case 0: attn_k<1><<<4096, 256, 0, stream>>>(Qb, Ks, Vs, ctxhi, ctxlo, al); break;
-      case 1: attn_k<2><<<4096, 256, 0, stream>>>(Qb, Ks, Vs, ctxhi, ctxlo, al); break;
-      case 2: attn_k<3><<<4096, 256, 0, stream>>>(Qb, Ks, Vs, ctxhi, ctxlo, al); break;
-      case 3: attn_k<4><<<4096, 256, 0, stream>>>(Qb, Ks, Vs, ctxhi, ctxlo, al); break;
-      case 4: attn_k<5><<<4096, 256, 0, stream>>>(Qb, Ks, Vs, ctxhi, ctxlo, al); break;
-      case 5: attn_k<6><<<4096, 256, 0, stream>>>(Qb, Ks, Vs, ctxhi, ctxlo, al); break;
-      case 6: attn_k<7><<<4096, 256, 0, stream>>>(Qb, Ks, Vs, ctxhi, ctxlo, al); break;
-      default: attn_k<8><<<4096, 256, 0, stream>>>(Qb, Ks, Vs, ctxhi, ctxlo, al); break;
-    }
-    gemm_ln<<<256, 512, 0, stream>>>(
-        ctxhi, ctxlo, HD, WoP, bo, lin1hi, lin1lo, ln1g, ln1b,
-        h1hi, h1lo, al);
-    ffn_ln<<<256, 512, 0, stream>>>(
-        h1hi, h1lo, Wf1P, bf1, Wf2P, bf2, ln2g, ln2b, hhhi, hhlo, al);
+      case 0: attn_wo_ln<1><<<256, 512, 0, stream>>>(Qb, Ks, Vs, WoP, bo, lin1hi, lin1lo, ln1g, ln1b, h1hi, h1lo, al); break;
+      case 1: attn_wo_ln<2><<<256, 512, 0, stream>>>(Qb, Ks, Vs, WoP, bo, lin1hi, lin1lo, ln1g, ln1b, h1hi, h1lo, al); break;
+      case 2: attn_wo_ln<3><<<256, 512, 0, stream>>>(Qb, Ks, Vs, WoP, bo, lin1hi, lin1lo, ln1g, ln1b, h1hi, h1lo, al); break;
+      case 3: attn_wo_ln<4><<<256, 512, 0, stream>>>(Qb, Ks, Vs, WoP, bo, lin1hi, lin1lo, ln1g, ln1b, h1hi, h1lo, al); break;
+      case 4: attn_wo_ln<5><<<256, 512, 0, stream>>>(Qb, Ks, Vs, WoP, bo, lin1hi, lin1lo, ln1g, ln1b, h1hi, h1lo, al); break;
+      case 5: attn_wo_ln<6><<<256, 512, 0, stream>>>(Qb, Ks, Vs, WoP, bo, lin1hi, lin1lo, ln1g, ln1b, h1hi, h1lo, al); break;
+      case 6: attn_wo_ln<7><<<256, 512, 0, stream>>>(Qb, Ks, Vs, WoP, bo, lin1hi, lin1lo, ln1g, ln1b, h1hi, h1lo, al); break;
+      default: attn_wo_ln<8><<<256, 512, 0, stream>>>(Qb, Ks, Vs, WoP, bo, lin1hi, lin1lo, ln1g, ln1b, h1hi, h1lo, al); break;
+    }
     if (ci == 0)
-      s1_act<1><<<256, 256, 0, stream>>>(
-          hhhi, hhlo, Ws1P, bs1, Ws2, bs2, psa, psb,
+      ffn_act<0><<<256, 512, 0, stream>>>(
+          h1hi, h1lo, Wf1P, bf1, Wf2P, bf2, ln2g, ln2b,
+          Ws1P, bs1, Ws2, bs2, psa, psb,
           cum, rem, still, pc, outhi, outlo, pcdst, nullptr, flags + 0);
     else if (ci < CH - 1)
-      s1_act<0><<<256, 256, 0, stream>>>(
-          hhhi, hhlo, Ws1P, bs1, Ws2, bs2, psa, psb,
+      ffn_act<1><<<256, 512, 0, stream>>>(
+          h1hi, h1lo, Wf1P, bf1, Wf2P, bf2, ln2g, ln2b,
+          Ws1P, bs1, Ws2, bs2, psa, psb,
           cum, rem, still, pc, outhi, outlo, pcdst, al, flags + ci);
     else
-      act_last<<<2048, 256, 0, stream>>>(
-          hhhi, hhlo, cum, rem, still, pc, outhi, outlo, pcdst, al);
+      ffn_act<2><<<256, 512, 0, stream>>>(
+          h1hi, h1lo, Wf1P, bf1, Wf2P, bf2, ln2g, ln2b,
+          Ws1P, bs1, Ws2, bs2, psa, psb,
+          cum, rem, still, pc, outhi, outlo, pcdst, al, nullptr);
   }
   gemm2<1><<<dim3(128, 6), 256, 0, stream>>>(
       outhi, outlo, HD, WoutP, b_out, (float*)d_out, FB, FB);
```
